# Optimization experiments

Measured on AMD Instinct MI355X. Metric: run time of the kernel, lower is better.

Reference implementation:

```python
import jax, jax.numpy as jnp
import numpy as np

B, H, KH, D, L = 32, 32, 8, 128, 4096  # batch, q heads, kv heads, head dim, kv len
G = H // KH                             # GQA group size
SCALE = 0.08838834764831845             # head_dim ** -0.5


def setup_inputs() -> dict:
    key = jax.random.key(0)
    ks = jax.random.split(key, 5)
    q = jax.random.normal(ks[0], (B, H, D), jnp.float32)
    k = jax.random.normal(ks[1], (B, KH, D), jnp.float32)
    v = jax.random.normal(ks[2], (B, KH, D), jnp.float32)
    k_cache = jax.random.normal(ks[3], (B * L, KH, D), jnp.float32)
    v_cache = jax.random.normal(ks[4], (B * L, KH, D), jnp.float32)
    # paged slot table: row b lists the flat cache slots holding seq b's tokens
    kv_indices = jnp.arange(B * L, dtype=jnp.int32).reshape(B, L)
    return {"q": q, "k": k, "v": v, "k_cache": k_cache, "v_cache": v_cache,
            "kv_indices": kv_indices}


def reference(q, k, v, k_cache, v_cache, kv_indices):
    # output_kv_indices: slot for the newly generated token of each sequence
    cache_loc = kv_indices[:, -1]
    # set_kv_cache: append new k/v token into the paged pool
    k_cache = k_cache.at[cache_loc].set(k)
    v_cache = v_cache.at[cache_loc].set(v)
    # paged gather of each sequence's cached K/V: [B, L, KH, D]
    k_seq = k_cache[kv_indices]
    v_seq = v_cache[kv_indices]
    # GQA: group q heads per kv head -> [B, KH, G, D]
    qg = q.reshape(B, KH, G, D)
    scores = jnp.einsum('bkgd,blkd->bkgl', qg, k_seq) * SCALE  # [B, KH, G, L]
    p = jax.nn.softmax(scores, axis=-1)
    o = jnp.einsum('bkgl,blkd->bkgd', p, v_seq)                # [B, KH, G, D]
    return o.reshape(B, H * D)
```

## Files before the change

### kernel.cpp

```cpp
#include <hip/hip_runtime.h>
#include <math.h>

#define BB 32
#define HH 32
#define KHH 8
#define DD 128
#define LL 4096
#define GG 4
#define SCALE 0.08838834764831845f

#define NTHREADS 512
#define NW 8
#define NIT (LL / (NW * 4))

__global__ __launch_bounds__(NTHREADS, 1)
void attn_decode(const float* __restrict__ q,
                 const float* __restrict__ knew,
                 const float* __restrict__ vnew,
                 const float* __restrict__ kc,
                 const float* __restrict__ vc,
                 const int* __restrict__ kvi,
                 float* __restrict__ out) {
  __shared__ int   lds_val[LL];
  __shared__ float o_lds[NW][GG][DD];
  __shared__ float m_lds[NW][GG];
  __shared__ float s_lds[NW][GG];
  __shared__ int   lds_loc[BB];

  const int tid  = threadIdx.x;
  const int b    = blockIdx.x & 31;
  const int kh   = blockIdx.x >> 5;
  const int w    = tid >> 6;
  const int lane = tid & 63;
  const int qid  = lane >> 4;
  const int i16  = lane & 15;

  if (tid < BB) lds_loc[tid] = kvi[tid * LL + (LL - 1)];
  __syncthreads();
  for (int l = tid; l < LL; l += NTHREADS) {
    int idx = kvi[b * LL + l];
    int val = idx;
#pragma unroll
    for (int j = 0; j < BB; ++j)
      if (lds_loc[j] == idx) val = -(j + 1);
    lds_val[l] = val;
  }
  __syncthreads();

  const int khq = kh * GG;
  float qf[GG][8];
#pragma unroll
  for (int g = 0; g < GG; ++g) {
    const float* qp = q + ((size_t)b * HH + (khq + g)) * DD + i16 * 8;
#pragma unroll
    for (int j = 0; j < 8; ++j) qf[g][j] = qp[j];
  }

  float m[GG], s[GG], o[GG][8];
#pragma unroll
  for (int g = 0; g < GG; ++g) {
    m[g] = -INFINITY; s[g] = 0.f;
#pragma unroll
    for (int j = 0; j < 8; ++j) o[g][j] = 0.f;
  }

  const size_t khoff = (size_t)kh * DD + i16 * 8;

  auto addr = [&](int it, const float*& kp, const float*& vp) {
    int l   = it * 32 + w * 4 + qid;
    int val = lds_val[l];
    int row = (val < 0) ? (-val - 1) : val;
    const float* kb = (val < 0) ? knew : kc;
    const float* vb = (val < 0) ? vnew : vc;
    size_t off = ((size_t)row * (KHH * DD)) + khoff;
    kp = kb + off;
    vp = vb + off;
  };

  const float *kp, *vp;
  addr(0, kp, vp);
  float4 ka  = *(const float4*)kp;
  float4 kb4 = *(const float4*)(kp + 4);
  float4 va  = *(const float4*)vp;
  float4 vb4 = *(const float4*)(vp + 4);

  for (int it = 0; it < NIT; ++it) {
    float4 nka, nkb, nva, nvb;
    if (it + 1 < NIT) {
      const float *nkp, *nvp;
      addr(it + 1, nkp, nvp);
      nka = *(const float4*)nkp;
      nkb = *(const float4*)(nkp + 4);
      nva = *(const float4*)nvp;
      nvb = *(const float4*)(nvp + 4);
    } else {
      nka = ka; nkb = kb4; nva = va; nvb = vb4;
    }

#pragma unroll
    for (int g = 0; g < GG; ++g) {
      float sc = qf[g][0]*ka.x  + qf[g][1]*ka.y  + qf[g][2]*ka.z  + qf[g][3]*ka.w
               + qf[g][4]*kb4.x + qf[g][5]*kb4.y + qf[g][6]*kb4.z + qf[g][7]*kb4.w;
#pragma unroll
      for (int msk = 1; msk < 16; msk <<= 1)
        sc += __shfl_xor(sc, msk);
      sc *= SCALE;

      if (sc > m[g]) {
        float so = __expf(m[g] - sc);
        m[g] = sc;
        s[g] *= so;
#pragma unroll
        for (int j = 0; j < 8; ++j) o[g][j] *= so;
      }
      float p = __expf(sc - m[g]);
      s[g] += p;
      o[g][0] += p * va.x;  o[g][1] += p * va.y;  o[g][2] += p * va.z;  o[g][3] += p * va.w;
      o[g][4] += p * vb4.x; o[g][5] += p * vb4.y; o[g][6] += p * vb4.z; o[g][7] += p * vb4.w;
    }

    ka = nka; kb4 = nkb; va = nva; vb4 = nvb;
  }

#pragma unroll
  for (int g = 0; g < GG; ++g) {
#pragma unroll
    for (int off = 16; off < 64; off <<= 1) {
      float m2 = __shfl_xor(m[g], off);
      float s2 = __shfl_xor(s[g], off);
      float M  = fmaxf(m[g], m2);
      float w1 = __expf(m[g] - M);
      float w2 = __expf(m2 - M);
      s[g] = w1 * s[g] + w2 * s2;
#pragma unroll
      for (int j = 0; j < 8; ++j) {
        float o2 = __shfl_xor(o[g][j], off);
        o[g][j] = w1 * o[g][j] + w2 * o2;
      }
      m[g] = M;
    }
  }

  if (lane < 16) {
#pragma unroll
    for (int g = 0; g < GG; ++g) {
#pragma unroll
      for (int j = 0; j < 8; ++j) o_lds[w][g][i16 * 8 + j] = o[g][j];
      if (lane == 0) { m_lds[w][g] = m[g]; s_lds[w][g] = s[g]; }
    }
  }
  __syncthreads();

  {
    int g = tid >> 7;
    int d = tid & 127;
    float M = -INFINITY;
#pragma unroll
    for (int wv = 0; wv < NW; ++wv) M = fmaxf(M, m_lds[wv][g]);
    float ss = 0.f, oo = 0.f;
#pragma unroll
    for (int wv = 0; wv < NW; ++wv) {
      float wt = __expf(m_lds[wv][g] - M);
      ss += wt * s_lds[wv][g];
      oo += wt * o_lds[wv][g][d];
    }
    out[((size_t)b * HH + (khq + g)) * DD + d] = oo / ss;
  }
}

extern "C" void kernel_launch(void* const* d_in, const int* in_sizes, int n_in,
                              void* d_out, int out_size, void* d_ws, size_t ws_size,
                              hipStream_t stream) {
  const float* q    = (const float*)d_in[0];
  const float* knew = (const float*)d_in[1];
  const float* vnew = (const float*)d_in[2];
  const float* kc   = (const float*)d_in[3];
  const float* vc   = (const float*)d_in[4];
  const int*   kvi  = (const int*)d_in[5];
  float* out = (float*)d_out;

  attn_decode<<<dim3(BB * KHH), dim3(NTHREADS), 0, stream>>>(q, knew, vnew, kc, vc, kvi, out);
}
```

Baseline: 190.6 us.

## Split KV length across blocks with all heads per block plus merge kernel

Replaces the one-block-per-(batch, kv-head) decode kernel with a split-KV scheme. Each block now covers one batch and a 512-token chunk across all 8 KV heads, reading full contiguous 4KB cache rows with 16-float vectors per lane. A second kernel merges the partial softmax states from the workspace. This is meant to improve memory coalescing and per-block index-table work, at the cost of an extra launch and workspace traffic. The old kernel is kept as a fallback when the workspace is too small.

```diff
diff --git a/kernel.cpp b/kernel.cpp
--- a/kernel.cpp
+++ b/kernel.cpp
@@ -11,16 +11,195 @@
 
 #define NTHREADS 512
 #define NW 8
-#define NIT (LL / (NW * 4))
-
+#define SPLITS 8
+#define RPB (LL / SPLITS)
+#define RPW (RPB / NW)
+
+#define WS_O_FLOATS   (BB * SPLITS * HH * DD)
+#define WS_MS_FLOATS  (BB * SPLITS * HH * 2)
+#define WS_NEED_BYTES ((size_t)(WS_O_FLOATS + WS_MS_FLOATS) * 4)
+
+typedef float f4 __attribute__((ext_vector_type(4)));
+
+__global__ __launch_bounds__(NTHREADS, 2)
+void attn_part(const float* __restrict__ q,
+               const float* __restrict__ knew,
+               const float* __restrict__ vnew,
+               const float* __restrict__ kc,
+               const float* __restrict__ vc,
+               const int* __restrict__ kvi,
+               float* __restrict__ ws_o,
+               float* __restrict__ ws_ms) {
+  __shared__ int   lds_val[RPB];
+  __shared__ int   lds_loc[BB];
+  __shared__ float o_lds[NW][KHH][GG][DD];
+  __shared__ float m_lds[NW][KHH][GG];
+  __shared__ float s_lds[NW][KHH][GG];
+
+  const int tid  = threadIdx.x;
+  const int b    = blockIdx.x >> 3;
+  const int sp   = blockIdx.x & 7;
+  const int w    = tid >> 6;
+  const int lane = tid & 63;
+  const int kh   = lane >> 3;
+  const int sub  = lane & 7;
+  const int d0   = sub * 16;
+
+  const int base = sp * RPB;
+
+  if (tid < BB) lds_loc[tid] = kvi[tid * LL + (LL - 1)];
+  __syncthreads();
+  {
+    int idx = kvi[b * LL + base + tid];
+    int val = idx;
+#pragma unroll
+    for (int j = 0; j < BB; ++j)
+      if (lds_loc[j] == idx) val = -(j + 1);
+    lds_val[tid] = val;
+  }
+  __syncthreads();
+
+  f4 qf[GG][4];
+#pragma unroll
+  for (int g = 0; g < GG; ++g) {
+    const float* qp = q + ((size_t)b * HH + (kh * GG + g)) * DD + d0;
+#pragma unroll
+    for (int c = 0; c < 4; ++c) qf[g][c] = *(const f4*)(qp + c * 4);
+  }
+
+  f4 o[GG][4];
+  float m[GG], sden[GG];
+#pragma unroll
+  for (int g = 0; g < GG; ++g) {
+    m[g] = -INFINITY; sden[g] = 0.f;
+#pragma unroll
+    for (int c = 0; c < 4; ++c) o[g][c] = (f4){0.f, 0.f, 0.f, 0.f};
+  }
+
+  auto addr = [&](int it, const float*& kp, const float*& vp) {
+    int l   = w * RPW + it;
+    int val = lds_val[l];
+    int row = (val < 0) ? (-val - 1) : val;
+    const float* kb = (val < 0) ? knew : kc;
+    const float* vb = (val < 0) ? vnew : vc;
+    size_t off = (size_t)row * (KHH * DD) + lane * 16;
+    kp = kb + off;
+    vp = vb + off;
+  };
+
+#define LOADKV(it, K0, K1, K2, K3, V0, V1, V2, V3)  \
+  { const float *kp_, *vp_; addr(it, kp_, vp_);     \
+    K0 = *(const f4*)kp_;        K1 = *(const f4*)(kp_ + 4);  \
+    K2 = *(const f4*)(kp_ + 8);  K3 = *(const f4*)(kp_ + 12); \
+    V0 = *(const f4*)vp_;        V1 = *(const f4*)(vp_ + 4);  \
+    V2 = *(const f4*)(vp_ + 8);  V3 = *(const f4*)(vp_ + 12); }
+
+  auto compute = [&](f4 k0, f4 k1, f4 k2, f4 k3,
+                     f4 v0, f4 v1, f4 v2, f4 v3) {
+    float sc[GG];
+#pragma unroll
+    for (int g = 0; g < GG; ++g) {
+      f4 t = qf[g][0] * k0 + qf[g][1] * k1 + qf[g][2] * k2 + qf[g][3] * k3;
+      float s1 = t[0] + t[1] + t[2] + t[3];
+#pragma unroll
+      for (int msk = 1; msk < 8; msk <<= 1)
+        s1 += __shfl_xor(s1, msk);
+      sc[g] = s1 * SCALE;
+    }
+#pragma unroll
+    for (int g = 0; g < GG; ++g) {
+      if (sc[g] > m[g]) {
+        float so = __expf(m[g] - sc[g]);
+        m[g] = sc[g];
+        sden[g] *= so;
+#pragma unroll
+        for (int c = 0; c < 4; ++c) o[g][c] *= so;
+      }
+      float p = __expf(sc[g] - m[g]);
+      sden[g] += p;
+      o[g][0] += p * v0; o[g][1] += p * v1; o[g][2] += p * v2; o[g][3] += p * v3;
+    }
+  };
+
+  f4 kA0, kA1, kA2, kA3, vA0, vA1, vA2, vA3;
+  f4 kB0, kB1, kB2, kB3, vB0, vB1, vB2, vB3;
+  LOADKV(0, kA0, kA1, kA2, kA3, vA0, vA1, vA2, vA3);
+#pragma unroll 1
+  for (int it = 0; it < RPW; it += 2) {
+    LOADKV(it + 1, kB0, kB1, kB2, kB3, vB0, vB1, vB2, vB3);
+    compute(kA0, kA1, kA2, kA3, vA0, vA1, vA2, vA3);
+    if (it + 2 < RPW) LOADKV(it + 2, kA0, kA1, kA2, kA3, vA0, vA1, vA2, vA3);
+    compute(kB0, kB1, kB2, kB3, vB0, vB1, vB2, vB3);
+  }
+
+#pragma unroll
+  for (int g = 0; g < GG; ++g)
+#pragma unroll
+    for (int c = 0; c < 4; ++c)
+      *(f4*)&o_lds[w][kh][g][d0 + c * 4] = o[g][c];
+  if (sub == 0) {
+#pragma unroll
+    for (int g = 0; g < GG; ++g) { m_lds[w][kh][g] = m[g]; s_lds[w][kh][g] = sden[g]; }
+  }
+  __syncthreads();
+
+#pragma unroll
+  for (int rep = 0; rep < (KHH * GG * DD) / NTHREADS; ++rep) {
+    int idx = rep * NTHREADS + tid;
+    int kh2 = idx >> 9;
+    int g2  = (idx >> 7) & 3;
+    int d   = idx & 127;
+    float M = -INFINITY;
+#pragma unroll
+    for (int wv = 0; wv < NW; ++wv) M = fmaxf(M, m_lds[wv][kh2][g2]);
+    float den = 0.f, num = 0.f;
+#pragma unroll
+    for (int wv = 0; wv < NW; ++wv) {
+      float wt = __expf(m_lds[wv][kh2][g2] - M);
+      den += wt * s_lds[wv][kh2][g2];
+      num += wt * o_lds[wv][kh2][g2][d];
+    }
+    int h    = kh2 * GG + g2;
+    int part = (b * SPLITS + sp) * HH + h;
+    ws_o[(size_t)part * DD + d] = num;
+    if (d == 0) { ws_ms[part * 2] = M; ws_ms[part * 2 + 1] = den; }
+  }
+}
+
+__global__ __launch_bounds__(NTHREADS)
+void attn_merge(const float* __restrict__ ws_o,
+                const float* __restrict__ ws_ms,
+                float* __restrict__ out) {
+  const int b  = blockIdx.x >> 3;
+  const int kh = blockIdx.x & 7;
+  const int g  = threadIdx.x >> 7;
+  const int d  = threadIdx.x & 127;
+  const int h  = kh * GG + g;
+
+  float M = -INFINITY;
+#pragma unroll
+  for (int s = 0; s < SPLITS; ++s)
+    M = fmaxf(M, ws_ms[((b * SPLITS + s) * HH + h) * 2]);
+  float den = 0.f, num = 0.f;
+#pragma unroll
+  for (int s = 0; s < SPLITS; ++s) {
+    int part = (b * SPLITS + s) * HH + h;
+    float wt = __expf(ws_ms[part * 2] - M);
+    den += wt * ws_ms[part * 2 + 1];
+    num += wt * ws_o[(size_t)part * DD + d];
+  }
+  out[((size_t)b * HH + h) * DD + d] = num / den;
+}
+
+#define FNIT (LL / (NW * 4))
 __global__ __launch_bounds__(NTHREADS, 1)
-void attn_decode(const float* __restrict__ q,
-                 const float* __restrict__ knew,
-                 const float* __restrict__ vnew,
-                 const float* __restrict__ kc,
-                 const float* __restrict__ vc,
-                 const int* __restrict__ kvi,
-                 float* __restrict__ out) {
+void attn_decode_fb(const float* __restrict__ q,
+                    const float* __restrict__ knew,
+                    const float* __restrict__ vnew,
+                    const float* __restrict__ kc,
+                    const float* __restrict__ vc,
+                    const int* __restrict__ kvi,
+                    float* __restrict__ out) {
   __shared__ int   lds_val[LL];
   __shared__ float o_lds[NW][GG][DD];
   __shared__ float m_lds[NW][GG];
@@ -28,8 +207,8 @@
   __shared__ int   lds_loc[BB];
 
   const int tid  = threadIdx.x;
-  const int b    = blockIdx.x & 31;
-  const int kh   = blockIdx.x >> 5;
+  const int b    = blockIdx.x >> 3;
+  const int kh   = blockIdx.x & 7;
   const int w    = tid >> 6;
   const int lane = tid & 63;
   const int qid  = lane >> 4;
@@ -65,7 +244,6 @@
   }
 
   const size_t khoff = (size_t)kh * DD + i16 * 8;
-
   auto addr = [&](int it, const float*& kp, const float*& vp) {
     int l   = it * 32 + w * 4 + qid;
     int val = lds_val[l];
@@ -73,8 +251,7 @@
     const float* kb = (val < 0) ? knew : kc;
     const float* vb = (val < 0) ? vnew : vc;
     size_t off = ((size_t)row * (KHH * DD)) + khoff;
-    kp = kb + off;
-    vp = vb + off;
+    kp = kb + off; vp = vb + off;
   };
 
   const float *kp, *vp;
@@ -84,32 +261,25 @@
   float4 va  = *(const float4*)vp;
   float4 vb4 = *(const float4*)(vp + 4);
 
-  for (int it = 0; it < NIT; ++it) {
+  for (int it = 0; it < FNIT; ++it) {
     float4 nka, nkb, nva, nvb;
-    if (it + 1 < NIT) {
+    if (it + 1 < FNIT) {
       const float *nkp, *nvp;
       addr(it + 1, nkp, nvp);
-      nka = *(const float4*)nkp;
-      nkb = *(const float4*)(nkp + 4);
-      nva = *(const float4*)nvp;
-      nvb = *(const float4*)(nvp + 4);
-    } else {
-      nka = ka; nkb = kb4; nva = va; nvb = vb4;
-    }
+      nka = *(const float4*)nkp; nkb = *(const float4*)(nkp + 4);
+      nva = *(const float4*)nvp; nvb = *(const float4*)(nvp + 4);
+    } else { nka = ka; nkb = kb4; nva = va; nvb = vb4; }
 
 #pragma unroll
     for (int g = 0; g < GG; ++g) {
       float sc = qf[g][0]*ka.x  + qf[g][1]*ka.y  + qf[g][2]*ka.z  + qf[g][3]*ka.w
                + qf[g][4]*kb4.x + qf[g][5]*kb4.y + qf[g][6]*kb4.z + qf[g][7]*kb4.w;
 #pragma unroll
-      for (int msk = 1; msk < 16; msk <<= 1)
-        sc += __shfl_xor(sc, msk);
+      for (int msk = 1; msk < 16; msk <<= 1) sc += __shfl_xor(sc, msk);
       sc *= SCALE;
-
       if (sc > m[g]) {
         float so = __expf(m[g] - sc);
-        m[g] = sc;
-        s[g] *= so;
+        m[g] = sc; s[g] *= so;
 #pragma unroll
         for (int j = 0; j < 8; ++j) o[g][j] *= so;
       }
@@ -118,7 +288,6 @@
       o[g][0] += p * va.x;  o[g][1] += p * va.y;  o[g][2] += p * va.z;  o[g][3] += p * va.w;
       o[g][4] += p * vb4.x; o[g][5] += p * vb4.y; o[g][6] += p * vb4.z; o[g][7] += p * vb4.w;
     }
-
     ka = nka; kb4 = nkb; va = nva; vb4 = nvb;
   }
 
@@ -150,7 +319,6 @@
     }
   }
   __syncthreads();
-
   {
     int g = tid >> 7;
     int d = tid & 127;
@@ -179,5 +347,14 @@
   const int*   kvi  = (const int*)d_in[5];
   float* out = (float*)d_out;
 
-  attn_decode<<<dim3(BB * KHH), dim3(NTHREADS), 0, stream>>>(q, knew, vnew, kc, vc, kvi, out);
+  if (ws_size >= WS_NEED_BYTES) {
+    float* ws_o  = (float*)d_ws;
+    float* ws_ms = ws_o + WS_O_FLOATS;
+    attn_part<<<dim3(BB * SPLITS), dim3(NTHREADS), 0, stream>>>(
+        q, knew, vnew, kc, vc, kvi, ws_o, ws_ms);
+    attn_merge<<<dim3(BB * KHH), dim3(NTHREADS), 0, stream>>>(ws_o, ws_ms, out);
+  } else {
+    attn_decode_fb<<<dim3(BB * KHH), dim3(NTHREADS), 0, stream>>>(
+        q, knew, vnew, kc, vc, kvi, out);
+  }
 }
```

After: 194.6 us. 2.1% more time.
